# Performance work log

Measured on AMD Instinct MI355X. Metric: run time of the kernel, lower is better.

The kernel has to match this reference:

```python
import jax, jax.numpy as jnp
import numpy as np

B, C, M, H, W = 4, 12, 2, 320, 320
TOL = 1e-6
MAX_ITER = 10


def to_c(t):
    # [..., 2] real -> complex
    return jax.lax.complex(t[..., 0], t[..., 1])


def to_r(t):
    return jnp.stack([jnp.real(t), jnp.imag(t)], axis=-1)


def fft2c(x):
    return jnp.fft.fft2(x, axes=(-2, -1), norm='ortho')


def ifft2c(x):
    return jnp.fft.ifft2(x, axes=(-2, -1), norm='ortho')


def A_op(x, sm, mk):
    # x: [B,M,H,W] complex, sm: [B,C,M,H,W] complex, mk: [B,C,H,W] real
    coil_imgs = jnp.sum(x[:, None] * sm, axis=2)  # [B,C,H,W]
    return fft2c(coil_imgs) * mk


def AT_op(y, sm, mk):
    img = ifft2c(y * mk)  # [B,C,H,W]
    return jnp.sum(jnp.conj(sm) * img[:, :, None], axis=1)  # [B,M,H,W]


def cg_solve(x0, Mop, tol=TOL, max_iter=MAX_ITER):
    b = x0.shape[0]
    x0x0 = jnp.sum(jnp.abs(x0.reshape(b, -1)) ** 2, axis=-1)  # [B] real

    def body(carry, _):
        x, r, p, rr = carry
        active = jnp.min(rr / x0x0) > tol  # tol check, gated like the while-loop
        q = Mop(p)
        pq = jnp.sum((p * jnp.conj(q)).reshape(b, -1), axis=-1)  # complexDot(p, q)
        alpha = rr.astype(x0.dtype) / pq  # complex_div(rr, <p,q>)
        a = alpha[:, None, None, None]
        x_new = x + a * p
        r_new = r - a * q
        rr_new = jnp.sum(jnp.abs(r_new.reshape(b, -1)) ** 2, axis=-1)
        beta = (rr_new / rr)[:, None, None, None].astype(x0.dtype)
        p_new = r_new + beta * p
        new = (x_new, r_new, p_new, rr_new)
        carry = jax.tree.map(lambda n, o: jnp.where(active, n, o), new, carry)
        return carry, None

    rr0 = jnp.sum(jnp.abs(x0.reshape(b, -1)) ** 2, axis=-1)
    init = (jnp.zeros_like(x0), x0, x0, rr0)
    (x, _, _, _), _ = jax.lax.scan(body, init, None, length=max_iter)
    return x


def setup_inputs() -> dict:
    key = jax.random.key(0)
    k1, k2, k3, k4 = jax.random.split(key, 4)
    x = jax.random.normal(k1, (B, M, H, W, 2), dtype=jnp.float32)
    y = jax.random.normal(k2, (B, C, H, W, 2), dtype=jnp.float32)
    smaps = jax.random.normal(k3, (B, C, M, H, W, 2), dtype=jnp.float32) * 0.2
    mask = jax.random.randint(k4, (B, C, H, W, 1), 0, 2).astype(jnp.float32)
    lambda_a = jnp.full((1,), 0.05, dtype=jnp.float32)
    return {"x": x, "y": y, "smaps": smaps, "mask": mask, "lambda_a": lambda_a}


def reference(x, y, smaps, mask, lambda_a):
    z = to_c(x)          # [B,M,H,W]
    yc = to_c(y)         # [B,C,H,W]
    sm = to_c(smaps)     # [B,C,M,H,W]
    mk = mask[..., 0]    # [B,C,H,W]
    lam = lambda_a[0]

    x0 = lam * AT_op(yc, sm, mk) + z

    def Mop(p):
        return lam * AT_op(A_op(p, sm, mk), sm, mk) + p

    return to_r(cg_solve(x0, Mop))
```

## Files before the change

kernel.cpp:

```cpp
#include <hip/hip_runtime.h>
#include <math.h>

#define NB 4
#define NC 12
#define NM 2
#define NN 320
#define NHW (NN*NN)
#define NBC (NB*NC)
#define CG_TOL 1e-6f
#define NITER 10
#define CBLK 400

#define TWO_PI_F 6.28318530717958647692f

typedef float2 c32;

__device__ __forceinline__ c32 cmul(c32 a, c32 b){ return make_float2(a.x*b.x - a.y*b.y, a.x*b.y + a.y*b.x); }
__device__ __forceinline__ c32 cmulj(c32 a, c32 b){ return make_float2(a.x*b.x + a.y*b.y, a.x*b.y - a.y*b.x); }
__device__ __forceinline__ c32 cadd(c32 a, c32 b){ return make_float2(a.x+b.x, a.y+b.y); }
__device__ __forceinline__ c32 csub(c32 a, c32 b){ return make_float2(a.x-b.x, a.y-b.y); }
__device__ __forceinline__ c32 cscale(c32 a, float s){ return make_float2(a.x*s, a.y*s); }

template<bool FWD>
__device__ __forceinline__ c32 twmul(c32 a, c32 t){
  return FWD ? make_float2(a.x*t.x + a.y*t.y, a.y*t.x - a.x*t.y)
             : make_float2(a.x*t.x - a.y*t.y, a.y*t.x + a.x*t.y);
}

__device__ __forceinline__ float wave_reduce_f(float v) {
  #pragma unroll
  for (int off = 32; off >= 1; off >>= 1) v += __shfl_xor(v, off, 64);
  return v;
}
__device__ __forceinline__ c32 wave_reduce_c(c32 v) {
  #pragma unroll
  for (int off = 32; off >= 1; off >>= 1) {
    v.x += __shfl_xor(v.x, off, 64);
    v.y += __shfl_xor(v.y, off, 64);
  }
  return v;
}

__global__ __launch_bounds__(256)
void twiddle_init(c32* __restrict__ T320, c32* __restrict__ T64)
{
  const int t = threadIdx.x;
  {
    float s, c; sincosf(TWO_PI_F * (float)t / 320.f, &s, &c);
    T320[t] = make_float2(c, s);
  }
  if (t < 32) {
    float s, c; sincosf(TWO_PI_F * (float)t / 64.f, &s, &c);
    T64[t] = make_float2(c, s);
  }
}

template<bool FWD>
__device__ __forceinline__ void radix5(c32 V[5]) {
  constexpr float C1 = 0.30901699437494745f;
  constexpr float S1 = 0.9510565162951535f;
  constexpr float C2 = -0.8090169943749475f;
  constexpr float S2 = 0.5877852522924731f;
  constexpr float sg = FWD ? -1.f : 1.f;
  const c32 w1 = make_float2(C1,  sg*S1);
  const c32 w2 = make_float2(C2,  sg*S2);
  const c32 w3 = make_float2(C2, -sg*S2);
  const c32 w4 = make_float2(C1, -sg*S1);
  c32 v0=V[0], v1=V[1], v2=V[2], v3=V[3], v4=V[4];
  V[0] = cadd(cadd(v0, v1), cadd(cadd(v2, v3), v4));
  V[1] = cadd(v0, cadd(cadd(cmul(v1,w1), cmul(v2,w2)), cadd(cmul(v3,w3), cmul(v4,w4))));
  V[2] = cadd(v0, cadd(cadd(cmul(v1,w2), cmul(v2,w4)), cadd(cmul(v3,w1), cmul(v4,w3))));
  V[3] = cadd(v0, cadd(cadd(cmul(v1,w3), cmul(v2,w1)), cadd(cmul(v3,w4), cmul(v4,w2))));
  V[4] = cadd(v0, cadd(cadd(cmul(v1,w4), cmul(v2,w3)), cadd(cmul(v3,w2), cmul(v4,w1))));
}

template<bool FWD>
__device__ __forceinline__ void fft320_x2(c32 A[5], c32 B[5],
                                          const c32 ct[4], const c32 tw[6], int lane)
{
  radix5<FWD>(A);
  radix5<FWD>(B);
  #pragma unroll
  for (int k = 1; k < 5; ++k) {
    A[k] = twmul<FWD>(A[k], ct[k-1]);
    B[k] = twmul<FWD>(B[k], ct[k-1]);
  }
  #pragma unroll
  for (int s = 0; s < 6; ++s) {
    const int m = 32 >> s;
    const c32 w = tw[s];
    const bool up = (lane & m) != 0;
    c32 oA[5], oB[5];
    #pragma unroll
    for (int k = 0; k < 5; ++k) { oA[k].x = __shfl_xor(A[k].x, m, 64); oA[k].y = __shfl_xor(A[k].y, m, 64); }
    #pragma unroll
    for (int k = 0; k < 5; ++k) { oB[k].x = __shfl_xor(B[k].x, m, 64); oB[k].y = __shfl_xor(B[k].y, m, 64); }
    #pragma unroll
    for (int k = 0; k < 5; ++k) {
      c32 loA = cadd(A[k], oA[k]);
      c32 hiA = twmul<FWD>(csub(oA[k], A[k]), w);
      A[k] = up ? hiA : loA;
      c32 loB = cadd(B[k], oB[k]);
      c32 hiB = twmul<FWD>(csub(oB[k], B[k]), w);
      B[k] = up ? hiB : loB;
    }
  }
}

#define LOAD_TWIDDLES \
  c32 ct[4], tw[6]; \
  _Pragma("unroll") for (int k_ = 0; k_ < 4; ++k_) ct[k_] = T320[(k_ + 1) * lane]; \
  _Pragma("unroll") for (int s_ = 0; s_ < 6; ++s_) tw[s_] = T64[(lane & ((32 >> s_) - 1)) << s_];

template<bool FWD, bool MASK_IN, bool NAT_OUT>
__global__ __launch_bounds__(256)
void fft_pass(const c32* __restrict__ in, c32* __restrict__ out,
              const float* __restrict__ mask, const float* __restrict__ flag,
              const c32* __restrict__ T320, const c32* __restrict__ T64)
{
  if (flag != nullptr && flag[0] == 0.f) return;
  __shared__ c32 tile[8][NN + 2];
  const int tid = threadIdx.x, lane = tid & 63, wv = tid >> 6;
  const int bc = blockIdx.y, r0 = blockIdx.x * 8;
  LOAD_TWIDDLES
  const int rv6 = __brev((unsigned)lane) >> 26;
  const int rA = r0 + wv*2, rB = rA + 1;
  c32 A[5], B[5];
  #pragma unroll
  for (int j = 0; j < 5; ++j) {
    const size_t iA = ((size_t)bc * NN + rA) * NN + lane + 64*j;
    const size_t iB = ((size_t)bc * NN + rB) * NN + lane + 64*j;
    A[j] = in[iA]; B[j] = in[iB];
    if constexpr (MASK_IN) { A[j] = cscale(A[j], mask[iA]); B[j] = cscale(B[j], mask[iB]); }
  }
  fft320_x2<FWD>(A, B, ct, tw, lane);
  #pragma unroll
  for (int k = 0; k < 5; ++k) {
    tile[wv*2    ][k + 5*rv6] = A[k];
    tile[wv*2 + 1][k + 5*rv6] = B[k];
  }
  __syncthreads();
  if constexpr (!NAT_OUT) {
    #pragma unroll
    for (int it = 0; it < 10; ++it) {
      const int idx = it * 256 + tid, u = idx >> 3, d = idx & 7;
      out[((size_t)bc * NN + u) * NN + (r0 + d)] = tile[d][u];
    }
  } else {
    #pragma unroll
    for (int it = 0; it < 10; ++it) {
      const int idx = it * 256 + tid, d = idx / NN, u = idx - d * NN;
      out[((size_t)bc * NN + (r0 + d)) * NN + u] = tile[d][u];
    }
  }
}

__global__ __launch_bounds__(256)
void fft_comb(c32* __restrict__ out, const c32* __restrict__ pin,
              const c32* __restrict__ rres, c32* __restrict__ pout,
              const c32* __restrict__ smaps,
              const float* __restrict__ rr_prev, const float* __restrict__ rr_cur,
              const float* __restrict__ flag,
              const c32* __restrict__ T320, const c32* __restrict__ T64)
{
  if (flag[0] == 0.f) return;
  __shared__ c32 tile[8][NN + 2];
  const int tid = threadIdx.x, lane = tid & 63, wv = tid >> 6;
  const int bc = blockIdx.y, r0 = blockIdx.x * 8;
  const int b = bc / NC, c = bc - b * NC;
  const bool upd = (rr_cur != nullptr);
  const float beta = upd ? rr_cur[b] / rr_prev[b] : 0.f;
  LOAD_TWIDDLES
  const int rv6 = __brev((unsigned)lane) >> 26;
  const int rA = r0 + wv*2, rB = rA + 1;
  const size_t m0 = (size_t)(b*NM + 0) * NHW, m1 = (size_t)(b*NM + 1) * NHW;
  const size_t s0o = (size_t)((b*NC + c)*NM + 0) * NHW, s1o = (size_t)((b*NC + c)*NM + 1) * NHW;
  c32 A[5], B[5];
  #pragma unroll
  for (int j = 0; j < 5; ++j) {
    const size_t hA = (size_t)rA * NN + lane + 64*j;
    const size_t hB = (size_t)rB * NN + lane + 64*j;
    c32 r0A = rres[m0 + hA], r1A = rres[m1 + hA];
    c32 r0B = rres[m0 + hB], r1B = rres[m1 + hB];
    c32 p0A, p1A, p0B, p1B;
    if (upd) {
      p0A = cadd(r0A, cscale(pin[m0 + hA], beta));
      p1A = cadd(r1A, cscale(pin[m1 + hA], beta));
      p0B = cadd(r0B, cscale(pin[m0 + hB], beta));
      p1B = cadd(r1B, cscale(pin[m1 + hB], beta));
      if (c == 0) {
        pout[m0 + hA] = p0A; pout[m1 + hA] = p1A;
        pout[m0 + hB] = p0B; pout[m1 + hB] = p1B;
      }
    } else {
      p0A = r0A; p1A = r1A; p0B = r0B; p1B = r1B;
    }
    A[j] = cadd(cmul(p0A, smaps[s0o + hA]), cmul(p1A, smaps[s1o + hA]));
    B[j] = cadd(cmul(p0B, smaps[s0o + hB]), cmul(p1B, smaps[s1o + hB]));
  }
  fft320_x2<true>(A, B, ct, tw, lane);
  #pragma unroll
  for (int k = 0; k < 5; ++k) {
    tile[wv*2    ][k + 5*rv6] = A[k];
    tile[wv*2 + 1][k + 5*rv6] = B[k];
  }
  __syncthreads();
  #pragma unroll
  for (int it = 0; it < 10; ++it) {
    const int idx = it * 256 + tid, u = idx >> 3, d = idx & 7;
    out[((size_t)bc * NN + u) * NN + (r0 + d)] = tile[d][u];
  }
}

__global__ __launch_bounds__(256)
void fft_mask_ifft(const c32* __restrict__ in, c32* __restrict__ out,
                   const float* __restrict__ mask, const float* __restrict__ flag,
                   const c32* __restrict__ T320, const c32* __restrict__ T64)
{
  if (flag[0] == 0.f) return;
  __shared__ c32 tile[8][NN + 2];
  const int tid = threadIdx.x, lane = tid & 63, wv = tid >> 6;
  const int bc = blockIdx.y, r0 = blockIdx.x * 8;
  LOAD_TWIDDLES
  const int rv6 = __brev((unsigned)lane) >> 26;
  const int rA = r0 + wv*2, rB = rA + 1;
  c32 A[5], B[5];
  #pragma unroll
  for (int j = 0; j < 5; ++j) {
    A[j] = in[((size_t)bc * NN + rA) * NN + lane + 64*j];
    B[j] = in[((size_t)bc * NN + rB) * NN + lane + 64*j];
  }
  fft320_x2<true>(A, B, ct, tw, lane);
  #pragma unroll
  for (int k = 0; k < 5; ++k) {
    const int kh = k + 5*rv6;
    A[k] = cscale(A[k], mask[(size_t)bc * NHW + (size_t)kh * NN + rA]);
    B[k] = cscale(B[k], mask[(size_t)bc * NHW + (size_t)kh * NN + rB]);
  }
  #pragma unroll
  for (int k = 0; k < 5; ++k) {
    tile[wv*2    ][k + 5*rv6] = A[k];
    tile[wv*2 + 1][k + 5*rv6] = B[k];
  }
  #pragma unroll
  for (int j = 0; j < 5; ++j) {
    A[j] = tile[wv*2    ][lane + 64*j];
    B[j] = tile[wv*2 + 1][lane + 64*j];
  }
  fft320_x2<false>(A, B, ct, tw, lane);
  #pragma unroll
  for (int k = 0; k < 5; ++k) {
    tile[wv*2    ][k + 5*rv6] = A[k];
    tile[wv*2 + 1][k + 5*rv6] = B[k];
  }
  __syncthreads();
  #pragma unroll
  for (int it = 0; it < 10; ++it) {
    const int idx = it * 256 + tid, u = idx >> 3, d = idx & 7;
    out[((size_t)bc * NN + u) * NN + (r0 + d)] = tile[d][u];
  }
}

__global__ __launch_bounds__(256)
void init_combine(const c32* __restrict__ img, const c32* __restrict__ smaps,
                  const c32* __restrict__ z, c32* __restrict__ x,
                  c32* __restrict__ r, c32* __restrict__ p,
                  const float* __restrict__ lam, float* __restrict__ part)
{
  const int b  = blockIdx.y;
  const int hw = blockIdx.x * 256 + threadIdx.x;
  const float l0 = lam[0] * (1.f / (float)NN);
  c32 a0 = make_float2(0.f,0.f), a1 = make_float2(0.f,0.f);
  #pragma unroll
  for (int c = 0; c < NC; ++c) {
    c32 iv = img[(size_t)(b*NC + c) * NHW + hw];
    c32 s0 = smaps[(size_t)((b*NC + c)*NM + 0) * NHW + hw];
    c32 s1 = smaps[(size_t)((b*NC + c)*NM + 1) * NHW + hw];
    a0 = cadd(a0, cmulj(s0, iv));
    a1 = cadd(a1, cmulj(s1, iv));
  }
  const size_t i0 = (size_t)(b*NM + 0) * NHW + hw;
  const size_t i1 = (size_t)(b*NM + 1) * NHW + hw;
  c32 x00 = cadd(cscale(a0, l0), z[i0]);
  c32 x01 = cadd(cscale(a1, l0), z[i1]);
  x[i0] = make_float2(0.f,0.f); x[i1] = make_float2(0.f,0.f);
  r[i0] = x00; r[i1] = x01;
  p[i0] = x00; p[i1] = x01;
  float acc = x00.x*x00.x + x00.y*x00.y + x01.x*x01.x + x01.y*x01.y;
  acc = wave_reduce_f(acc);
  __shared__ float sred[4];
  const int lane = threadIdx.x & 63, wv = threadIdx.x >> 6;
  if (lane == 0) sred[wv] = acc;
  __syncthreads();
  if (threadIdx.x == 0) part[b*CBLK + blockIdx.x] = sred[0]+sred[1]+sred[2]+sred[3];
}

__global__ void reduce_init(const float* __restrict__ part, float* __restrict__ x0x0,
                            float* __restrict__ rr0, float* __restrict__ flags)
{
  const int lane = threadIdx.x & 63;
  const int b = threadIdx.x >> 6;
  float s = 0.f;
  for (int j = lane; j < CBLK; j += 64) s += part[b*CBLK + j];
  s = wave_reduce_f(s);
  if (lane == 0) { x0x0[b] = s; rr0[b] = s; }
  if (threadIdx.x == 0) flags[0] = 1.f;
}

__global__ __launch_bounds__(256)
void q_combine(const c32* __restrict__ img, const c32* __restrict__ smaps,
               const c32* __restrict__ p, c32* __restrict__ q,
               const float* __restrict__ lam, const float* __restrict__ flag,
               c32* __restrict__ pqpart)
{
  if (flag[0] == 0.f) return;
  const int b  = blockIdx.y;
  const int hw = blockIdx.x * 256 + threadIdx.x;
  const float lq = lam[0] * (1.f / (float)NHW);
  c32 a0 = make_float2(0.f,0.f), a1 = make_float2(0.f,0.f);
  #pragma unroll
  for (int c = 0; c < NC; ++c) {
    c32 iv = img[(size_t)(b*NC + c) * NHW + hw];
    c32 s0 = smaps[(size_t)((b*NC + c)*NM + 0) * NHW + hw];
    c32 s1 = smaps[(size_t)((b*NC + c)*NM + 1) * NHW + hw];
    a0 = cadd(a0, cmulj(s0, iv));
    a1 = cadd(a1, cmulj(s1, iv));
  }
  const size_t i0 = (size_t)(b*NM + 0) * NHW + hw;
  const size_t i1 = (size_t)(b*NM + 1) * NHW + hw;
  c32 p0 = p[i0], p1 = p[i1];
  c32 q0 = cadd(cscale(a0, lq), p0);
  c32 q1 = cadd(cscale(a1, lq), p1);
  q[i0] = q0; q[i1] = q1;
  c32 s = cadd(cmulj(q0, p0), cmulj(q1, p1));
  s = wave_reduce_c(s);
  __shared__ c32 sred[4];
  const int lane = threadIdx.x & 63, wv = threadIdx.x >> 6;
  if (lane == 0) sred[wv] = s;
  __syncthreads();
  if (threadIdx.x == 0)
    pqpart[b*CBLK + blockIdx.x] = cadd(cadd(sred[0], sred[1]), cadd(sred[2], sred[3]));
}

__global__ __launch_bounds__(256)
void update1(c32* __restrict__ x, c32* __restrict__ r,
             const c32* __restrict__ p, const c32* __restrict__ q,
             const float* __restrict__ rr_i, const c32* __restrict__ pqpart,
             const float* __restrict__ flag, float* __restrict__ part)
{
  if (flag[0] == 0.f) return;
  const int b = blockIdx.y;
  const int t = threadIdx.x;
  c32 s = make_float2(0.f, 0.f);
  for (int j = t; j < CBLK; j += 256) s = cadd(s, pqpart[b*CBLK + j]);
  s = wave_reduce_c(s);
  __shared__ c32 spq[4];
  const int lane = t & 63, wv = t >> 6;
  if (lane == 0) spq[wv] = s;
  __syncthreads();
  const c32 pqv = cadd(cadd(spq[0], spq[1]), cadd(spq[2], spq[3]));
  const float rrv = rr_i[b];
  const float den = pqv.x*pqv.x + pqv.y*pqv.y;
  const c32 alpha = make_float2(rrv * pqv.x / den, -rrv * pqv.y / den);
  const int hw = blockIdx.x * 256 + t;
  float acc = 0.f;
  #pragma unroll
  for (int m = 0; m < NM; ++m) {
    const size_t idx = (size_t)(b*NM + m) * NHW + hw;
    c32 pe = p[idx], qe = q[idx];
    c32 xe = cadd(x[idx], cmul(alpha, pe));
    c32 re = csub(r[idx], cmul(alpha, qe));
    x[idx] = xe; r[idx] = re;
    acc += re.x*re.x + re.y*re.y;
  }
  acc = wave_reduce_f(acc);
  __shared__ float sred[4];
  if (lane == 0) sred[wv] = acc;
  __syncthreads();
  if (t == 0) part[b*CBLK + blockIdx.x] = sred[0]+sred[1]+sred[2]+sred[3];
}

__global__ void reduce_rr(const float* __restrict__ part, const float* __restrict__ rr_i,
                          float* __restrict__ rr_n, const float* __restrict__ x0x0,
                          const float* __restrict__ flag_i, float* __restrict__ flag_n)
{
  const int lane = threadIdx.x & 63;
  const int b = threadIdx.x >> 6;
  __shared__ float sred[4];
  __shared__ float sx0[4];
  if (flag_i[0] == 0.f) {
    if (lane == 0) rr_n[b] = rr_i[b];
    if (threadIdx.x == 0) flag_n[0] = 0.f;
    return;
  }
  float s = 0.f;
  for (int j = lane; j < CBLK; j += 64) s += part[b*CBLK + j];
  s = wave_reduce_f(s);
  if (lane == 0) { rr_n[b] = s; sred[b] = s; sx0[b] = x0x0[b]; }
  __syncthreads();
  if (threadIdx.x == 0) {
    float mn = 1e30f;
    #pragma unroll
    for (int bb = 0; bb < NB; ++bb) mn = fminf(mn, sred[bb] / sx0[bb]);
    flag_n[0] = (mn > CG_TOL) ? 1.f : 0.f;
  }
}

extern "C" void kernel_launch(void* const* d_in, const int* in_sizes, int n_in,
                              void* d_out, int out_size, void* d_ws, size_t ws_size,
                              hipStream_t stream)
{
  const c32*  z   = (const c32*)d_in[0];
  const c32*  y   = (const c32*)d_in[1];
  const c32*  sm  = (const c32*)d_in[2];
  const float* mk = (const float*)d_in[3];
  const float* lam= (const float*)d_in[4];
  c32* x = (c32*)d_out;

  char* base = (char*)d_ws;
  size_t off = 0;
  auto walloc = [&](size_t bytes) -> void* {
    void* ptr = base + off;
    off += (bytes + 255) & ~(size_t)255;
    return ptr;
  };
  c32* buf1   = (c32*)walloc((size_t)NBC * NHW * sizeof(c32));
  c32* buf2   = (c32*)walloc((size_t)NBC * NHW * sizeof(c32));
  c32* rv     = (c32*)walloc((size_t)NB * NM * NHW * sizeof(c32));
  c32* pvA    = (c32*)walloc((size_t)NB * NM * NHW * sizeof(c32));
  c32* pvB    = (c32*)walloc((size_t)NB * NM * NHW * sizeof(c32));
  c32* qv     = (c32*)walloc((size_t)NB * NM * NHW * sizeof(c32));
  c32* pqpart = (c32*)walloc((size_t)NB * CBLK * sizeof(c32));
  float* x0x0 = (float*)walloc(NB * sizeof(float));
  float* rr   = (float*)walloc((NITER + 1) * NB * sizeof(float));
  float* flags= (float*)walloc((NITER + 1) * sizeof(float));
  float* part1= (float*)walloc((size_t)NB * CBLK * sizeof(float));
  c32* T320   = (c32*)walloc(256 * sizeof(c32));
  c32* T64    = (c32*)walloc(32 * sizeof(c32));
  (void)ws_size; (void)in_sizes; (void)n_in; (void)out_size;

  dim3 fgrid(NN / 8, NBC), blk(256);
  dim3 cgrid(CBLK, NB);

  twiddle_init<<<1, 256, 0, stream>>>(T320, T64);

  fft_pass<false, true,  false><<<fgrid, blk, 0, stream>>>(y,    buf2, mk,      nullptr, T320, T64);
  fft_pass<false, false, false><<<fgrid, blk, 0, stream>>>(buf2, buf1, nullptr, nullptr, T320, T64);
  init_combine<<<cgrid, blk, 0, stream>>>(buf1, sm, z, x, rv, pvA, lam, part1);
  reduce_init<<<1, 256, 0, stream>>>(part1, x0x0, rr, flags);

  for (int i = 0; i < NITER; ++i) {
    const float* fl = flags + i;
    c32* pin  = (i & 1) ? pvA : pvB;
    c32* pout = (i & 1) ? pvB : pvA;
    const float* rrprev = (i > 0) ? (rr + (i-1)*NB) : rr;
    const float* rrcur  = (i > 0) ? (rr + i*NB) : nullptr;
    fft_comb<<<fgrid, blk, 0, stream>>>(buf2, pin, rv, pout, sm, rrprev, rrcur, fl, T320, T64);
    fft_mask_ifft<<<fgrid, blk, 0, stream>>>(buf2, buf1, mk, fl, T320, T64);
    fft_pass<false, false, true><<<fgrid, blk, 0, stream>>>(buf1, buf2, nullptr, fl, T320, T64);
    q_combine<<<cgrid, blk, 0, stream>>>(buf2, sm, pout, qv, lam, fl, pqpart);
    update1<<<cgrid, blk, 0, stream>>>(x, rv, pout, qv, rr + i*NB, pqpart, fl, part1);
    reduce_rr<<<1, 256, 0, stream>>>(part1, rr + i*NB, rr + (i+1)*NB, x0x0, fl, flags + (i+1));
  }
}
```

Measured before the change: 398.9 us.

## Fuse final inverse FFT pass with coil combine and fold residual reductions into fft_comb

The last inverse FFT row pass and the q_combine coil sum become one kernel, ifft_q. Each block transforms one image row for all 12 coils, with each wave handling 3 coils. It accumulates conj(smap)·image in registers, reduces across waves in shared memory, and writes q and the partial <p,q> directly, so the full multi-coil intermediate buffer is no longer written and re-read. The reduce_init and reduce_rr single-block kernels are removed: every fft_comb block now reduces the rr partials and recomputes the convergence flag and beta itself, cutting kernel launches and serial dependencies. The cost is redundant reduction work in every block, some duplicated global writes of rr and flags, and lower parallelism in the fused ifft_q kernel.

Result: faster. 377.3 us (-5.4%).

```diff
diff --git a/kernel.cpp b/kernel.cpp
--- a/kernel.cpp
+++ b/kernel.cpp
@@ -9,7 +9,10 @@
 #define NBC (NB*NC)
 #define CG_TOL 1e-6f
 #define NITER 10
-#define CBLK 400
+#define PBLK 400
+#define QBLK 320
+#define QROW 4
+#define LSTR (NN + 2)
 
 #define TWO_PI_F 6.28318530717958647692f
 
@@ -21,10 +24,10 @@
 __device__ __forceinline__ c32 csub(c32 a, c32 b){ return make_float2(a.x-b.x, a.y-b.y); }
 __device__ __forceinline__ c32 cscale(c32 a, float s){ return make_float2(a.x*s, a.y*s); }
 
-template<bool FWD>
+template<bool CONJ>
 __device__ __forceinline__ c32 twmul(c32 a, c32 t){
-  return FWD ? make_float2(a.x*t.x + a.y*t.y, a.y*t.x - a.x*t.y)
-             : make_float2(a.x*t.x - a.y*t.y, a.y*t.x + a.x*t.y);
+  return CONJ ? make_float2(a.x*t.x + a.y*t.y, a.y*t.x - a.x*t.y)
+              : make_float2(a.x*t.x - a.y*t.y, a.y*t.x + a.x*t.y);
 }
 
 __device__ __forceinline__ float wave_reduce_f(float v) {
@@ -107,19 +110,41 @@
   }
 }
 
+template<bool FWD>
+__device__ __forceinline__ void fft320_one(c32 A[5], const c32 ct[4], const c32 tw[6], int lane)
+{
+  radix5<FWD>(A);
+  #pragma unroll
+  for (int k = 1; k < 5; ++k) A[k] = twmul<FWD>(A[k], ct[k-1]);
+  #pragma unroll
+  for (int s = 0; s < 6; ++s) {
+    const int m = 32 >> s;
+    const c32 w = tw[s];
+    const bool up = (lane & m) != 0;
+    c32 o[5];
+    #pragma unroll
+    for (int k = 0; k < 5; ++k) { o[k].x = __shfl_xor(A[k].x, m, 64); o[k].y = __shfl_xor(A[k].y, m, 64); }
+    #pragma unroll
+    for (int k = 0; k < 5; ++k) {
+      c32 lo = cadd(A[k], o[k]);
+      c32 hi = twmul<FWD>(csub(o[k], A[k]), w);
+      A[k] = up ? hi : lo;
+    }
+  }
+}
+
 #define LOAD_TWIDDLES \
   c32 ct[4], tw[6]; \
   _Pragma("unroll") for (int k_ = 0; k_ < 4; ++k_) ct[k_] = T320[(k_ + 1) * lane]; \
   _Pragma("unroll") for (int s_ = 0; s_ < 6; ++s_) tw[s_] = T64[(lane & ((32 >> s_) - 1)) << s_];
 
-template<bool FWD, bool MASK_IN, bool NAT_OUT>
+template<bool FWD, bool MASK_IN>
 __global__ __launch_bounds__(256)
 void fft_pass(const c32* __restrict__ in, c32* __restrict__ out,
-              const float* __restrict__ mask, const float* __restrict__ flag,
+              const float* __restrict__ mask,
               const c32* __restrict__ T320, const c32* __restrict__ T64)
 {
-  if (flag != nullptr && flag[0] == 0.f) return;
-  __shared__ c32 tile[8][NN + 2];
+  __shared__ c32 tile[8][LSTR];
   const int tid = threadIdx.x, lane = tid & 63, wv = tid >> 6;
   const int bc = blockIdx.y, r0 = blockIdx.x * 8;
   LOAD_TWIDDLES
@@ -140,36 +165,81 @@
     tile[wv*2 + 1][k + 5*rv6] = B[k];
   }
   __syncthreads();
-  if constexpr (!NAT_OUT) {
-    #pragma unroll
-    for (int it = 0; it < 10; ++it) {
-      const int idx = it * 256 + tid, u = idx >> 3, d = idx & 7;
-      out[((size_t)bc * NN + u) * NN + (r0 + d)] = tile[d][u];
-    }
-  } else {
-    #pragma unroll
-    for (int it = 0; it < 10; ++it) {
-      const int idx = it * 256 + tid, d = idx / NN, u = idx - d * NN;
-      out[((size_t)bc * NN + (r0 + d)) * NN + u] = tile[d][u];
-    }
-  }
+  #pragma unroll
+  for (int it = 0; it < 10; ++it) {
+    const int idx = it * 256 + tid, u = idx >> 3, d = idx & 7;
+    out[((size_t)bc * NN + u) * NN + (r0 + d)] = tile[d][u];
+  }
+}
+
+__global__ __launch_bounds__(256)
+void init_combine(const c32* __restrict__ img, const c32* __restrict__ smaps,
+                  const c32* __restrict__ z, c32* __restrict__ x,
+                  c32* __restrict__ r, c32* __restrict__ p,
+                  const float* __restrict__ lam, float* __restrict__ part)
+{
+  const int b  = blockIdx.y;
+  const int hw = blockIdx.x * 256 + threadIdx.x;
+  const float l0 = lam[0] * (1.f / (float)NN);
+  c32 a0 = make_float2(0.f,0.f), a1 = make_float2(0.f,0.f);
+  #pragma unroll
+  for (int c = 0; c < NC; ++c) {
+    c32 iv = img[(size_t)(b*NC + c) * NHW + hw];
+    c32 s0 = smaps[(size_t)((b*NC + c)*NM + 0) * NHW + hw];
+    c32 s1 = smaps[(size_t)((b*NC + c)*NM + 1) * NHW + hw];
+    a0 = cadd(a0, cmulj(s0, iv));
+    a1 = cadd(a1, cmulj(s1, iv));
+  }
+  const size_t i0 = (size_t)(b*NM + 0) * NHW + hw;
+  const size_t i1 = (size_t)(b*NM + 1) * NHW + hw;
+  c32 x00 = cadd(cscale(a0, l0), z[i0]);
+  c32 x01 = cadd(cscale(a1, l0), z[i1]);
+  x[i0] = make_float2(0.f,0.f); x[i1] = make_float2(0.f,0.f);
+  r[i0] = x00; r[i1] = x01;
+  p[i0] = x00; p[i1] = x01;
+  float acc = x00.x*x00.x + x00.y*x00.y + x01.x*x01.x + x01.y*x01.y;
+  acc = wave_reduce_f(acc);
+  __shared__ float sred[4];
+  const int lane = threadIdx.x & 63, wv = threadIdx.x >> 6;
+  if (lane == 0) sred[wv] = acc;
+  __syncthreads();
+  if (threadIdx.x == 0) part[b*PBLK + blockIdx.x] = sred[0]+sred[1]+sred[2]+sred[3];
 }
 
 __global__ __launch_bounds__(256)
 void fft_comb(c32* __restrict__ out, const c32* __restrict__ pin,
               const c32* __restrict__ rres, c32* __restrict__ pout,
               const c32* __restrict__ smaps,
-              const float* __restrict__ rr_prev, const float* __restrict__ rr_cur,
-              const float* __restrict__ flag,
+              float* __restrict__ rr, float* __restrict__ flags,
+              const float* __restrict__ part1, const int it,
               const c32* __restrict__ T320, const c32* __restrict__ T64)
 {
-  if (flag[0] == 0.f) return;
-  __shared__ c32 tile[8][NN + 2];
+  __shared__ c32 tile[8][LSTR];
+  __shared__ float sstat[NB];
   const int tid = threadIdx.x, lane = tid & 63, wv = tid >> 6;
   const int bc = blockIdx.y, r0 = blockIdx.x * 8;
   const int b = bc / NC, c = bc - b * NC;
-  const bool upd = (rr_cur != nullptr);
-  const float beta = upd ? rr_cur[b] / rr_prev[b] : 0.f;
+  {
+    float s = 0.f;
+    for (int j = lane; j < PBLK; j += 64) s += part1[wv*PBLK + j];
+    s = wave_reduce_f(s);
+    if (lane == 0) sstat[wv] = s;
+  }
+  __syncthreads();
+  float flag;
+  if (it == 0) flag = 1.f;
+  else {
+    float mn = 1e30f;
+    #pragma unroll
+    for (int bb = 0; bb < NB; ++bb) mn = fminf(mn, sstat[bb] / rr[bb]);
+    flag = (mn > CG_TOL) ? 1.f : 0.f;
+  }
+  if (tid < NB) rr[it*NB + tid] = sstat[tid];
+  if (tid == 0) flags[it] = flag;
+  if (it != 0 && flag == 0.f) return;
+  const float beta = (it != 0) ? sstat[b] / rr[(it-1)*NB + b] : 0.f;
+  const bool upd = (it != 0);
+
   LOAD_TWIDDLES
   const int rv6 = __brev((unsigned)lane) >> 26;
   const int rA = r0 + wv*2, rB = rA + 1;
@@ -206,8 +276,8 @@
   }
   __syncthreads();
   #pragma unroll
-  for (int it = 0; it < 10; ++it) {
-    const int idx = it * 256 + tid, u = idx >> 3, d = idx & 7;
+  for (int it5 = 0; it5 < 10; ++it5) {
+    const int idx = it5 * 256 + tid, u = idx >> 3, d = idx & 7;
     out[((size_t)bc * NN + u) * NN + (r0 + d)] = tile[d][u];
   }
 }
@@ -218,7 +288,7 @@
                    const c32* __restrict__ T320, const c32* __restrict__ T64)
 {
   if (flag[0] == 0.f) return;
-  __shared__ c32 tile[8][NN + 2];
+  __shared__ c32 tile[8][LSTR];
   const int tid = threadIdx.x, lane = tid & 63, wv = tid >> 6;
   const int bc = blockIdx.y, r0 = blockIdx.x * 8;
   LOAD_TWIDDLES
@@ -262,104 +332,110 @@
 }
 
 __global__ __launch_bounds__(256)
-void init_combine(const c32* __restrict__ img, const c32* __restrict__ smaps,
-                  const c32* __restrict__ z, c32* __restrict__ x,
-                  c32* __restrict__ r, c32* __restrict__ p,
-                  const float* __restrict__ lam, float* __restrict__ part)
-{
-  const int b  = blockIdx.y;
-  const int hw = blockIdx.x * 256 + threadIdx.x;
-  const float l0 = lam[0] * (1.f / (float)NN);
-  c32 a0 = make_float2(0.f,0.f), a1 = make_float2(0.f,0.f);
-  #pragma unroll
-  for (int c = 0; c < NC; ++c) {
-    c32 iv = img[(size_t)(b*NC + c) * NHW + hw];
-    c32 s0 = smaps[(size_t)((b*NC + c)*NM + 0) * NHW + hw];
-    c32 s1 = smaps[(size_t)((b*NC + c)*NM + 1) * NHW + hw];
-    a0 = cadd(a0, cmulj(s0, iv));
-    a1 = cadd(a1, cmulj(s1, iv));
-  }
-  const size_t i0 = (size_t)(b*NM + 0) * NHW + hw;
-  const size_t i1 = (size_t)(b*NM + 1) * NHW + hw;
-  c32 x00 = cadd(cscale(a0, l0), z[i0]);
-  c32 x01 = cadd(cscale(a1, l0), z[i1]);
-  x[i0] = make_float2(0.f,0.f); x[i1] = make_float2(0.f,0.f);
-  r[i0] = x00; r[i1] = x01;
-  p[i0] = x00; p[i1] = x01;
-  float acc = x00.x*x00.x + x00.y*x00.y + x01.x*x01.x + x01.y*x01.y;
-  acc = wave_reduce_f(acc);
-  __shared__ float sred[4];
-  const int lane = threadIdx.x & 63, wv = threadIdx.x >> 6;
-  if (lane == 0) sred[wv] = acc;
-  __syncthreads();
-  if (threadIdx.x == 0) part[b*CBLK + blockIdx.x] = sred[0]+sred[1]+sred[2]+sred[3];
-}
-
-__global__ void reduce_init(const float* __restrict__ part, float* __restrict__ x0x0,
-                            float* __restrict__ rr0, float* __restrict__ flags)
-{
-  const int lane = threadIdx.x & 63;
-  const int b = threadIdx.x >> 6;
-  float s = 0.f;
-  for (int j = lane; j < CBLK; j += 64) s += part[b*CBLK + j];
-  s = wave_reduce_f(s);
-  if (lane == 0) { x0x0[b] = s; rr0[b] = s; }
-  if (threadIdx.x == 0) flags[0] = 1.f;
-}
-
-__global__ __launch_bounds__(256)
-void q_combine(const c32* __restrict__ img, const c32* __restrict__ smaps,
-               const c32* __restrict__ p, c32* __restrict__ q,
-               const float* __restrict__ lam, const float* __restrict__ flag,
-               c32* __restrict__ pqpart)
+void ifft_q(const c32* __restrict__ bufin, const c32* __restrict__ smaps,
+            const c32* __restrict__ p, c32* __restrict__ q,
+            const float* __restrict__ lam, const float* __restrict__ flag,
+            c32* __restrict__ pqpart,
+            const c32* __restrict__ T320, const c32* __restrict__ T64)
 {
   if (flag[0] == 0.f) return;
-  const int b  = blockIdx.y;
-  const int hw = blockIdx.x * 256 + threadIdx.x;
+  __shared__ c32 tile[QROW][LSTR];
+  const int tid = threadIdx.x, lane = tid & 63, wv = tid >> 6;
+  const int b = blockIdx.y, h = blockIdx.x;
+  LOAD_TWIDDLES
+  const int rv6 = __brev((unsigned)lane) >> 26;
   const float lq = lam[0] * (1.f / (float)NHW);
-  c32 a0 = make_float2(0.f,0.f), a1 = make_float2(0.f,0.f);
-  #pragma unroll
-  for (int c = 0; c < NC; ++c) {
-    c32 iv = img[(size_t)(b*NC + c) * NHW + hw];
-    c32 s0 = smaps[(size_t)((b*NC + c)*NM + 0) * NHW + hw];
-    c32 s1 = smaps[(size_t)((b*NC + c)*NM + 1) * NHW + hw];
-    a0 = cadd(a0, cmulj(s0, iv));
-    a1 = cadd(a1, cmulj(s1, iv));
-  }
-  const size_t i0 = (size_t)(b*NM + 0) * NHW + hw;
-  const size_t i1 = (size_t)(b*NM + 1) * NHW + hw;
-  c32 p0 = p[i0], p1 = p[i1];
-  c32 q0 = cadd(cscale(a0, lq), p0);
-  c32 q1 = cadd(cscale(a1, lq), p1);
-  q[i0] = q0; q[i1] = q1;
-  c32 s = cadd(cmulj(q0, p0), cmulj(q1, p1));
-  s = wave_reduce_c(s);
-  __shared__ c32 sred[4];
-  const int lane = threadIdx.x & 63, wv = threadIdx.x >> 6;
-  if (lane == 0) sred[wv] = s;
-  __syncthreads();
-  if (threadIdx.x == 0)
-    pqpart[b*CBLK + blockIdx.x] = cadd(cadd(sred[0], sred[1]), cadd(sred[2], sred[3]));
+  const size_t rowoff = (size_t)h * NN + lane;
+  c32 acc0[5], acc1[5];
+  #pragma unroll
+  for (int j = 0; j < 5; ++j) { acc0[j] = make_float2(0.f,0.f); acc1[j] = make_float2(0.f,0.f); }
+
+  for (int cc = 0; cc < 3; ++cc) {
+    const int c = wv * 3 + cc;
+    const size_t ib  = (size_t)(b*NC + c) * NHW + rowoff;
+    const size_t is0 = (size_t)((b*NC + c)*NM + 0) * NHW + rowoff;
+    const size_t is1 = (size_t)((b*NC + c)*NM + 1) * NHW + rowoff;
+    c32 A[5], S0[5], S1[5];
+    #pragma unroll
+    for (int j = 0; j < 5; ++j) {
+      A[j] = bufin[ib + 64*j]; S0[j] = smaps[is0 + 64*j]; S1[j] = smaps[is1 + 64*j];
+    }
+    fft320_one<false>(A, ct, tw, lane);
+    #pragma unroll
+    for (int k = 0; k < 5; ++k) tile[wv][k + 5*rv6] = A[k];
+    #pragma unroll
+    for (int j = 0; j < 5; ++j) {
+      c32 v = tile[wv][lane + 64*j];
+      acc0[j] = cadd(acc0[j], cmulj(S0[j], v));
+      acc1[j] = cadd(acc1[j], cmulj(S1[j], v));
+    }
+  }
+  c32* red = &tile[0][0];
+  __syncthreads();
+  if (wv >= 2) {
+    const int base = (wv - 2) * 640;
+    #pragma unroll
+    for (int j = 0; j < 5; ++j) {
+      red[base + j*64 + lane] = acc0[j];
+      red[base + 320 + j*64 + lane] = acc1[j];
+    }
+  }
+  __syncthreads();
+  if (wv < 2) {
+    const int base = wv * 640;
+    #pragma unroll
+    for (int j = 0; j < 5; ++j) {
+      acc0[j] = cadd(acc0[j], red[base + j*64 + lane]);
+      acc1[j] = cadd(acc1[j], red[base + 320 + j*64 + lane]);
+    }
+  }
+  __syncthreads();
+  if (wv == 1) {
+    #pragma unroll
+    for (int j = 0; j < 5; ++j) {
+      red[j*64 + lane] = acc0[j];
+      red[320 + j*64 + lane] = acc1[j];
+    }
+  }
+  __syncthreads();
+  if (wv == 0) {
+    const size_t i0 = (size_t)(b*NM + 0) * NHW + rowoff;
+    const size_t i1 = (size_t)(b*NM + 1) * NHW + rowoff;
+    c32 pqs = make_float2(0.f, 0.f);
+    #pragma unroll
+    for (int j = 0; j < 5; ++j) {
+      acc0[j] = cadd(acc0[j], red[j*64 + lane]);
+      acc1[j] = cadd(acc1[j], red[320 + j*64 + lane]);
+      c32 p0 = p[i0 + 64*j], p1 = p[i1 + 64*j];
+      c32 q0 = cadd(cscale(acc0[j], lq), p0);
+      c32 q1 = cadd(cscale(acc1[j], lq), p1);
+      q[i0 + 64*j] = q0; q[i1 + 64*j] = q1;
+      pqs = cadd(pqs, cadd(cmulj(q0, p0), cmulj(q1, p1)));
+    }
+    pqs = wave_reduce_c(pqs);
+    if (lane == 0) pqpart[b*QBLK + h] = pqs;
+  }
 }
 
 __global__ __launch_bounds__(256)
 void update1(c32* __restrict__ x, c32* __restrict__ r,
              const c32* __restrict__ p, const c32* __restrict__ q,
-             const float* __restrict__ rr_i, const c32* __restrict__ pqpart,
-             const float* __restrict__ flag, float* __restrict__ part)
+             const float* __restrict__ rr, const c32* __restrict__ pqpart,
+             const float* __restrict__ flag, float* __restrict__ part,
+             const int it)
 {
   if (flag[0] == 0.f) return;
   const int b = blockIdx.y;
   const int t = threadIdx.x;
   c32 s = make_float2(0.f, 0.f);
-  for (int j = t; j < CBLK; j += 256) s = cadd(s, pqpart[b*CBLK + j]);
+  for (int j = t; j < QBLK; j += 256) s = cadd(s, pqpart[b*QBLK + j]);
   s = wave_reduce_c(s);
   __shared__ c32 spq[4];
   const int lane = t & 63, wv = t >> 6;
   if (lane == 0) spq[wv] = s;
   __syncthreads();
   const c32 pqv = cadd(cadd(spq[0], spq[1]), cadd(spq[2], spq[3]));
-  const float rrv = rr_i[b];
+  const float rrv = rr[it*NB + b];
   const float den = pqv.x*pqv.x + pqv.y*pqv.y;
   const c32 alpha = make_float2(rrv * pqv.x / den, -rrv * pqv.y / den);
   const int hw = blockIdx.x * 256 + t;
@@ -377,33 +453,7 @@
   __shared__ float sred[4];
   if (lane == 0) sred[wv] = acc;
   __syncthreads();
-  if (t == 0) part[b*CBLK + blockIdx.x] = sred[0]+sred[1]+sred[2]+sred[3];
-}
-
-__global__ void reduce_rr(const float* __restrict__ part, const float* __restrict__ rr_i,
-                          float* __restrict__ rr_n, const float* __restrict__ x0x0,
-                          const float* __restrict__ flag_i, float* __restrict__ flag_n)
-{
-  const int lane = threadIdx.x & 63;
-  const int b = threadIdx.x >> 6;
-  __shared__ float sred[4];
-  __shared__ float sx0[4];
-  if (flag_i[0] == 0.f) {
-    if (lane == 0) rr_n[b] = rr_i[b];
-    if (threadIdx.x == 0) flag_n[0] = 0.f;
-    return;
-  }
-  float s = 0.f;
-  for (int j = lane; j < CBLK; j += 64) s += part[b*CBLK + j];
-  s = wave_reduce_f(s);
-  if (lane == 0) { rr_n[b] = s; sred[b] = s; sx0[b] = x0x0[b]; }
-  __syncthreads();
-  if (threadIdx.x == 0) {
-    float mn = 1e30f;
-    #pragma unroll
-    for (int bb = 0; bb < NB; ++bb) mn = fminf(mn, sred[bb] / sx0[bb]);
-    flag_n[0] = (mn > CG_TOL) ? 1.f : 0.f;
-  }
+  if (t == 0) part[b*PBLK + blockIdx.x] = sred[0]+sred[1]+sred[2]+sred[3];
 }
 
 extern "C" void kernel_launch(void* const* d_in, const int* in_sizes, int n_in,
@@ -430,36 +480,31 @@
   c32* pvA    = (c32*)walloc((size_t)NB * NM * NHW * sizeof(c32));
   c32* pvB    = (c32*)walloc((size_t)NB * NM * NHW * sizeof(c32));
   c32* qv     = (c32*)walloc((size_t)NB * NM * NHW * sizeof(c32));
-  c32* pqpart = (c32*)walloc((size_t)NB * CBLK * sizeof(c32));
-  float* x0x0 = (float*)walloc(NB * sizeof(float));
+  c32* pqpart = (c32*)walloc((size_t)NB * QBLK * sizeof(c32));
   float* rr   = (float*)walloc((NITER + 1) * NB * sizeof(float));
   float* flags= (float*)walloc((NITER + 1) * sizeof(float));
-  float* part1= (float*)walloc((size_t)NB * CBLK * sizeof(float));
+  float* part1= (float*)walloc((size_t)NB * PBLK * sizeof(float));
   c32* T320   = (c32*)walloc(256 * sizeof(c32));
   c32* T64    = (c32*)walloc(32 * sizeof(c32));
   (void)ws_size; (void)in_sizes; (void)n_in; (void)out_size;
 
-  dim3 fgrid(NN / 8, NBC), blk(256);
-  dim3 cgrid(CBLK, NB);
-
-  twiddle_init<<<1, 256, 0, stream>>>(T320, T64);
-
-  fft_pass<false, true,  false><<<fgrid, blk, 0, stream>>>(y,    buf2, mk,      nullptr, T320, T64);
-  fft_pass<false, false, false><<<fgrid, blk, 0, stream>>>(buf2, buf1, nullptr, nullptr, T320, T64);
-  init_combine<<<cgrid, blk, 0, stream>>>(buf1, sm, z, x, rv, pvA, lam, part1);
-  reduce_init<<<1, 256, 0, stream>>>(part1, x0x0, rr, flags);
+  dim3 blk256(256);
+  dim3 fgrid(NN / 8, NBC);
+  dim3 qgrid(QBLK, NB);
+  dim3 ugrid(PBLK, NB);
+
+  twiddle_init<<<1, blk256, 0, stream>>>(T320, T64);
+
+  fft_pass<false, true ><<<fgrid, blk256, 0, stream>>>(y,    buf2, mk,      T320, T64);
+  fft_pass<false, false><<<fgrid, blk256, 0, stream>>>(buf2, buf1, nullptr, T320, T64);
+  init_combine<<<ugrid, blk256, 0, stream>>>(buf1, sm, z, x, rv, pvA, lam, part1);
 
   for (int i = 0; i < NITER; ++i) {
-    const float* fl = flags + i;
     c32* pin  = (i & 1) ? pvA : pvB;
     c32* pout = (i & 1) ? pvB : pvA;
-    const float* rrprev = (i > 0) ? (rr + (i-1)*NB) : rr;
-    const float* rrcur  = (i > 0) ? (rr + i*NB) : nullptr;
-    fft_comb<<<fgrid, blk, 0, stream>>>(buf2, pin, rv, pout, sm, rrprev, rrcur, fl, T320, T64);
-    fft_mask_ifft<<<fgrid, blk, 0, stream>>>(buf2, buf1, mk, fl, T320, T64);
-    fft_pass<false, false, true><<<fgrid, blk, 0, stream>>>(buf1, buf2, nullptr, fl, T320, T64);
-    q_combine<<<cgrid, blk, 0, stream>>>(buf2, sm, pout, qv, lam, fl, pqpart);
-    update1<<<cgrid, blk, 0, stream>>>(x, rv, pout, qv, rr + i*NB, pqpart, fl, part1);
-    reduce_rr<<<1, 256, 0, stream>>>(part1, rr + i*NB, rr + (i+1)*NB, x0x0, fl, flags + (i+1));
-  }
-}
+    fft_comb<<<fgrid, blk256, 0, stream>>>(buf2, pin, rv, pout, sm, rr, flags, part1, i, T320, T64);
+    fft_mask_ifft<<<fgrid, blk256, 0, stream>>>(buf2, buf1, mk, flags + i, T320, T64);
+    ifft_q<<<qgrid, blk256, 0, stream>>>(buf1, sm, pout, qv, lam, flags + i, pqpart, T320, T64);
+    update1<<<ugrid, blk256, 0, stream>>>(x, rv, pout, qv, rr, pqpart, flags + i, part1, i);
+  }
+}
```
